# Kernel optimization log

Hardware: AMD Instinct MI355X
Metric: run time of the kernel (lower is better)

## Reference

```python
import jax, jax.numpy as jnp
import numpy as np
from jax import lax

D_MODEL = 96; D_STATE = 16; D_INNER = 192; DT_RANK = 6; K = 4
BSZ = 2; HH = 64; WW = 64


def setup_inputs() -> dict:
    key = jax.random.key(0)
    ks = jax.random.split(key, 16)
    f = lambda k, shape, s=0.02: (jax.random.normal(k, shape) * s).astype(jnp.float32)
    P = DT_RANK + 2 * D_STATE
    return {
        "x": jax.random.normal(ks[0], (BSZ, HH, WW, D_MODEL), jnp.float32),
        "W_in": f(ks[1], (2 * D_INNER, D_MODEL)),
        "b_in": jnp.zeros((2 * D_INNER,), jnp.float32),
        "conv_w": f(ks[2], (D_INNER, 1, 3, 3)),
        "conv_b": jnp.zeros((D_INNER,), jnp.float32),
        "W_xp": f(ks[3], (K * P, K * D_INNER)),
        "b_xp": jnp.zeros((K * P,), jnp.float32),
        "W_dt": f(ks[4], (K * D_INNER, K * DT_RANK)),
        "b_dt": f(ks[5], (K * D_INNER,), 0.1),
        "A_log": jax.random.normal(ks[6], (K * D_INNER, D_STATE), jnp.float32),
        "D_skip": jnp.ones((K * D_INNER,), jnp.float32),
        "dt_bias": jax.random.normal(ks[7], (K * D_INNER,), jnp.float32),
        "W_out": f(ks[8], (D_MODEL, D_INNER)),
        "b_out": jnp.zeros((D_MODEL,), jnp.float32),
        "gamma": jnp.ones((D_INNER,), jnp.float32),
        "beta": jnp.zeros((D_INNER,), jnp.float32),
    }


def cross_scan(x):
    # x: (B, D, H, W) -> (B, 4, D, L); dirs: row-major, col-major, and their reverses
    B, D, H, W = x.shape
    L = H * W
    x0 = x.reshape(B, D, L)
    x1 = jnp.swapaxes(x, 2, 3).reshape(B, D, L)
    return jnp.stack([x0, x1, x0[..., ::-1], x1[..., ::-1]], axis=1)


def cross_merge(ys):
    # ys: (B, 4, D, H, W) -> (B, D, L); inverse of cross_scan, summed
    B, Kk, D, H, W = ys.shape
    L = H * W
    yf = ys.reshape(B, Kk, D, L)
    y02 = yf[:, 0] + yf[:, 2, :, ::-1]
    y13 = yf[:, 1] + yf[:, 3, :, ::-1]
    y13 = jnp.swapaxes(y13.reshape(B, D, W, H), 2, 3).reshape(B, D, L)
    return y02 + y13


def selective_scan(u, dt, A, Bm, Cm, D_skip, dt_bias):
    # u, dt: (B,K,Dv,L); A: (K,Dv,N); Bm, Cm: (B,K,N,L); D_skip, dt_bias: (K,Dv)
    # NOTE: torch code repeats Bm/Cm across Dv; we broadcast instead (same math).
    dt = jax.nn.softplus(dt + dt_bias[None, :, :, None])
    dt_l = jnp.moveaxis(dt, -1, 0)   # (L,B,K,Dv)
    u_l = jnp.moveaxis(u, -1, 0)     # (L,B,K,Dv)
    B_l = jnp.moveaxis(Bm, -1, 0)    # (L,B,K,N)
    C_l = jnp.moveaxis(Cm, -1, 0)    # (L,B,K,N)

    def step(h, inp):
        dt_t, u_t, b_t, c_t = inp
        dA = jnp.exp(dt_t[..., None] * A[None])                 # (B,K,Dv,N)
        dBu = (dt_t * u_t)[..., None] * b_t[:, :, None, :]      # (B,K,Dv,N)
        h = dA * h + dBu
        y = jnp.einsum('bkdn,bkn->bkd', h, c_t)
        return h, y

    h0 = jnp.zeros(u.shape[:3] + (A.shape[-1],), u.dtype)
    _, ys = lax.scan(step, h0, (dt_l, u_l, B_l, C_l))
    ys = jnp.moveaxis(ys, 0, -1)  # (B,K,Dv,L)
    return ys + u * D_skip[None, :, :, None]


def reference(x, W_in, b_in, conv_w, conv_b, W_xp, b_xp, W_dt, b_dt,
              A_log, D_skip, dt_bias, W_out, b_out, gamma, beta):
    B, H, W, _ = x.shape
    L = H * W
    xz = x @ W_in.T + b_in
    xx, z = jnp.split(xz, 2, axis=-1)
    z = jax.nn.silu(z)
    xc = jnp.transpose(xx, (0, 3, 1, 2))  # (B, D, H, W)
    xc = lax.conv_general_dilated(xc, conv_w, (1, 1), 'SAME',
                                  feature_group_count=D_INNER,
                                  dimension_numbers=('NCHW', 'OIHW', 'NCHW'))
    xc = jax.nn.silu(xc + conv_b[None, :, None, None])

    xs = cross_scan(xc)                      # (B, K, D, L)
    xs_flat = xs.reshape(B, K * D_INNER, L)

    x_dbl = jnp.einsum('bcl,pc->bpl', xs_flat, W_xp) + b_xp[None, :, None]
    x_dbl = x_dbl.reshape(B, K, DT_RANK + 2 * D_STATE, L)
    dts, Bm, Cm = jnp.split(x_dbl, [DT_RANK, DT_RANK + D_STATE], axis=2)
    dts = dts.reshape(B, K * DT_RANK, L)
    dts = jnp.einsum('brl,dr->bdl', dts, W_dt) + b_dt[None, :, None]

    A = -jnp.exp(A_log).reshape(K, D_INNER, D_STATE)
    u = xs_flat.reshape(B, K, D_INNER, L)
    dt = dts.reshape(B, K, D_INNER, L)
    ys = selective_scan(u, dt, A, Bm, Cm,
                        D_skip.reshape(K, D_INNER), dt_bias.reshape(K, D_INNER))

    y = cross_merge(ys.reshape(B, K, D_INNER, H, W))  # (B, D, L)
    y = jnp.transpose(y.reshape(B, D_INNER, H, W), (0, 2, 3, 1))

    mu = jnp.mean(y, axis=-1, keepdims=True)
    var = jnp.mean(jnp.square(y - mu), axis=-1, keepdims=True)
    y = (y - mu) * lax.rsqrt(var + 1e-5) * gamma + beta
    y = y * z
    return y @ W_out.T + b_out
```

## Files before the change

kernel.cpp:

```cpp
#include <hip/hip_runtime.h>
#include <cstdint>
#include <cstddef>


#define CHUNK 16
#define NCK   256

#if __has_builtin(__builtin_amdgcn_exp2f)
#define EXP2(x) __builtin_amdgcn_exp2f(x)
#else
#define EXP2(x) exp2f(x)
#endif
#define LOG2E 1.44269504088896340736f
#define LN2   0.69314718055994530942f

typedef __attribute__((ext_vector_type(8))) short short8;
typedef __attribute__((ext_vector_type(8))) unsigned short ushort8;
typedef __attribute__((ext_vector_type(4))) float f32x4;

__device__ __forceinline__ float siluf(float x){ return x * (1.f/(1.f+__expf(-x))); }
__device__ __forceinline__ float softplus_fast(float v){
  float e  = EXP2(v*LOG2E);
  float sp = LN2*__log2f(1.f + e);
  return (v > 20.f) ? v : sp;
}
__device__ __forceinline__ unsigned short f2b(float f){
  uint32_t u = __float_as_uint(f);
  uint32_t r = (u + 0x7fffu + ((u>>16)&1u)) >> 16;
  return (unsigned short)r;
}
__device__ __forceinline__ short8 cast8(const float* p){
  float4 f0 = *(const float4*)p;
  float4 f1 = *(const float4*)(p+4);
  unsigned short t[8] = {f2b(f0.x),f2b(f0.y),f2b(f0.z),f2b(f0.w),
                         f2b(f1.x),f2b(f1.y),f2b(f1.z),f2b(f1.w)};
  return *(short8*)t;
}

__global__ __launch_bounds__(256) void k_pack(
    const float* __restrict__ Wxp, const float* __restrict__ Win,
    const float* __restrict__ Wout,
    unsigned short* __restrict__ Wf, unsigned short* __restrict__ Wfin,
    unsigned short* __restrict__ Wfout)
{
  int tid = blockIdx.x*256 + threadIdx.x;
  int lane = tid & 63;
  int n = lane & 15, q = lane >> 4;
  if (tid < 18432){
    int rest = tid >> 6;
    int pt = rest % 6; rest /= 6;
    int k32 = rest & 3; rest >>= 2;
    int kc = rest % 6; int ph = rest / 6;
    int p = ph*96 + pt*16 + n;
    int kbase = kc*128 + k32*32 + q*8;
    unsigned short v[8];
#pragma unroll
    for (int j = 0; j < 8; j++)
      v[j] = (p < 152) ? f2b(Wxp[(size_t)p*768 + kbase + j]) : (unsigned short)0;
    *(ushort8*)(Wf + (size_t)tid*8) = *(ushort8*)v;
  } else if (tid < 23040){
    int e = tid - 18432;
    int rest = e >> 6;
    int nt = rest % 24, k32 = rest / 24;
    int p = nt*16 + n;
    int kbase = k32*32 + q*8;
    unsigned short v[8];
#pragma unroll
    for (int j = 0; j < 8; j++) v[j] = f2b(Win[(size_t)p*96 + kbase + j]);
    *(ushort8*)(Wfin + (size_t)e*8) = *(ushort8*)v;
  } else if (tid < 25344){
    int e = tid - 23040;
    int rest = e >> 6;
    int nt = rest % 6, k32 = rest / 6;
    int p = nt*16 + n;
    int kbase = k32*32 + q*8;
    unsigned short v[8];
#pragma unroll
    for (int j = 0; j < 8; j++) v[j] = f2b(Wout[(size_t)p*192 + kbase + j]);
    *(ushort8*)(Wfout + (size_t)e*8) = *(ushort8*)v;
  }
}

__global__ __launch_bounds__(256) void k_gemm_in(
    const float* __restrict__ x, const unsigned short* __restrict__ Wfin,
    const float* __restrict__ bias, float* __restrict__ xx, float* __restrict__ zs)
{
  const int tid = threadIdx.x;
  const int lane = tid & 63, w = tid >> 6;
  const int m0 = blockIdx.x*64;
  const int n = lane & 15, q = lane >> 4;
  f32x4 acc[4][6] = {};
#pragma unroll
  for (int k32 = 0; k32 < 3; k32++){
    int kb = k32*32 + q*8;
    short8 a[4];
#pragma unroll
    for (int mf = 0; mf < 4; mf++)
      a[mf] = cast8(x + (size_t)(m0 + mf*16 + n)*96 + kb);
#pragma unroll
    for (int j = 0; j < 6; j++){
      int nt = w*6 + j;
      short8 bfr = *(const short8*)(Wfin + ((size_t)(k32*24 + nt)*64 + lane)*8);
#pragma unroll
      for (int mf = 0; mf < 4; mf++)
        acc[mf][j] = __builtin_amdgcn_mfma_f32_16x16x32_bf16(a[mf], bfr, acc[mf][j], 0, 0, 0);
    }
  }
#pragma unroll
  for (int mf = 0; mf < 4; mf++)
#pragma unroll
    for (int j = 0; j < 6; j++){
      int nn = w*96 + j*16 + n;
      float bv = bias[nn];
#pragma unroll
      for (int reg = 0; reg < 4; reg++){
        int l = m0 + mf*16 + q*4 + reg;
        float v = acc[mf][j][reg] + bv;
        if (nn < 192) xx[(size_t)l*192 + nn] = v;
        else          zs[(size_t)l*192 + (nn-192)] = siluf(v);
      }
    }
}

__global__ __launch_bounds__(256) void k_conv(
    const float* __restrict__ xx, const float* __restrict__ cw, const float* __restrict__ cb,
    float* __restrict__ xc,
    unsigned short* __restrict__ xcb, unsigned short* __restrict__ xcTb)
{
  int gid = blockIdx.x*256 + threadIdx.x;
  int c = gid % 192;
  int l = (gid/192) & 4095;
  int b = gid / (192*4096);
  int h = l >> 6, w = l & 63;
  float s = 0.f;
#pragma unroll
  for (int kh = 0; kh < 3; kh++){
    int h2 = h + kh - 1;
    if ((unsigned)h2 >= 64u) continue;
#pragma unroll
    for (int kw = 0; kw < 3; kw++){
      int w2 = w + kw - 1;
      if ((unsigned)w2 >= 64u) continue;
      s += xx[((size_t)b*4096 + h2*64 + w2)*192 + c] * cw[c*9 + kh*3 + kw];
    }
  }
  s = siluf(s + cb[c]);
  unsigned short sb = f2b(s);
  size_t i0 = ((size_t)b*4096 + l)*192 + c;
  xc[i0] = s; xcb[i0] = sb;
  int tl = (l & 63)*64 + (l >> 6);
  xcTb[((size_t)b*4096 + tl)*192 + c] = sb;
}

__global__ __launch_bounds__(256) void k_gemm_xdbl(
    const unsigned short* __restrict__ xcb, const unsigned short* __restrict__ xcTb,
    const unsigned short* __restrict__ Wf, const float* __restrict__ bxp,
    float* __restrict__ xdbl, float* __restrict__ dts_c)
{
  __shared__ unsigned short Bsh[4*6*64*8];
  const int tid = threadIdx.x;
  const int lane = tid & 63, w = tid >> 6;
  const int wl = w & 1, wp = w >> 1;
  const int l0 = blockIdx.x*64, ph = blockIdx.y, b = blockIdx.z;
  const int n = lane & 15, q = lane >> 4;
  f32x4 acc[2][3] = {};
  const unsigned short* slab0 = Wf + (size_t)ph*6*12288;
  for (int kc = 0; kc < 6; kc++){
    __syncthreads();
    const ushort8* srcp = (const ushort8*)(slab0 + (size_t)kc*12288);
#pragma unroll
    for (int t = 0; t < 6; t++) ((ushort8*)Bsh)[tid + t*256] = srcp[tid + t*256];
    __syncthreads();
#pragma unroll
    for (int k32 = 0; k32 < 4; k32++){
      int kk = kc*128 + k32*32;
      int dir = kk/192; int ch = kk%192 + q*8;
      const unsigned short* sp = (dir & 1) ? xcTb : xcb;
      bool rev = (dir >= 2);
      short8 a[2];
#pragma unroll
      for (int mt = 0; mt < 2; mt++){
        int ls = l0 + wl*32 + mt*16 + n;
        int row = rev ? 4095 - ls : ls;
        a[mt] = *(const short8*)(sp + ((size_t)b*4096 + row)*192 + ch);
      }
#pragma unroll
      for (int j = 0; j < 3; j++){
        short8 bfr = *(const short8*)&Bsh[((size_t)(k32*6 + wp*3 + j)*64 + lane)*8];
#pragma unroll
        for (int mt = 0; mt < 2; mt++)
          acc[mt][j] = __builtin_amdgcn_mfma_f32_16x16x32_bf16(a[mt], bfr, acc[mt][j], 0, 0, 0);
      }
    }
  }
#pragma unroll
  for (int mt = 0; mt < 2; mt++)
#pragma unroll
    for (int j = 0; j < 3; j++){
      int p = ph*96 + (wp*3+j)*16 + n;
      if (p < 152){
        int k = p/38, pp = p%38;
        int off = (pp < 6) ? pp : pp + 2;
        float bias = bxp[p];
#pragma unroll
        for (int reg = 0; reg < 4; reg++){
          int l = l0 + wl*32 + mt*16 + q*4 + reg;
          float val = acc[mt][j][reg] + bias;
          xdbl[(((size_t)b*4 + k)*4096 + l)*48 + off] = val;
          if (pp < 6) dts_c[((size_t)b*4096 + l)*24 + k*6 + pp] = val;
        }
      }
    }
}

__global__ __launch_bounds__(256) void k_scanA(
    const float* __restrict__ xc, const float* __restrict__ xdbl,
    const float* __restrict__ dts_c,
    const float* __restrict__ A_log, const float* __restrict__ Wdt,
    const float* __restrict__ bdt, const float* __restrict__ dtbias,
    float* __restrict__ dte, float* __restrict__ Pb, float* __restrict__ Sb)
{
  const int lane = threadIdx.x & 63;
  const int wid  = __builtin_amdgcn_readfirstlane(blockIdx.x*4 + (threadIdx.x >> 6));
  const int ck = wid & (NCK-1); const int g = wid / NCK;
  const int dblk = g % 3; const int bk = g / 3;
  const int k = bk & 3; const int b = bk >> 2;
  const int d = dblk*64 + lane; const int ch = k*192 + d;
  float An[16];
  {
    const float4* ap = (const float4*)(A_log + (size_t)ch*16);
#pragma unroll
    for (int i = 0; i < 4; i++){
      float4 t = ap[i];
      An[4*i+0] = -LOG2E*__expf(t.x); An[4*i+1] = -LOG2E*__expf(t.y);
      An[4*i+2] = -LOG2E*__expf(t.z); An[4*i+3] = -LOG2E*__expf(t.w);
    }
  }
  float Wr[24];
#pragma unroll
  for (int r = 0; r < 24; r++) Wr[r] = Wdt[(size_t)ch*24 + r];
  const float bsum = bdt[ch] + dtbias[ch];
  const int l0 = ck*CHUNK;
  const bool rev = (k >= 2);
  const int tr = k & 1;
  const int T0 = tr ? ((l0 & 63)*64 + (l0 >> 6)) : l0;
  const int rs = tr ? 64 : 1;
  const int row0 = rev ? 4095 - T0 : T0;
  const int rstep = (rev ? -rs : rs)*192;
  const float* up  = xc + ((size_t)b*4096 + row0)*192 + d;
  const float* qc  = dts_c + ((size_t)b*4096 + l0)*24;
  const float* xbc = xdbl + (((size_t)b*4 + k)*4096 + l0)*48;
  float* dtw = dte + (((size_t)b*4 + k)*4096 + l0)*192 + d;
  float h[16];
#pragma unroll
  for (int n = 0; n < 16; n++) h[n] = 0.f;
  float sdt = 0.f;
#pragma unroll 4
  for (int t = 0; t < CHUNK; t++){
    float u  = up[0];
    float4 B0 = *(const float4*)(xbc + 8);
    float4 B1 = *(const float4*)(xbc + 12);
    float4 B2 = *(const float4*)(xbc + 16);
    float4 B3 = *(const float4*)(xbc + 20);
    float Bv[16] = {B0.x,B0.y,B0.z,B0.w, B1.x,B1.y,B1.z,B1.w,
                    B2.x,B2.y,B2.z,B2.w, B3.x,B3.y,B3.z,B3.w};
    float4 q0 = *(const float4*)(qc);
    float4 q1 = *(const float4*)(qc + 4);
    float4 q2 = *(const float4*)(qc + 8);
    float4 q3 = *(const float4*)(qc + 12);
    float4 q4 = *(const float4*)(qc + 16);
    float4 q5 = *(const float4*)(qc + 20);
    float qv[24] = {q0.x,q0.y,q0.z,q0.w, q1.x,q1.y,q1.z,q1.w,
                    q2.x,q2.y,q2.z,q2.w, q3.x,q3.y,q3.z,q3.w,
                    q4.x,q4.y,q4.z,q4.w, q5.x,q5.y,q5.z,q5.w};
    float v0 = bsum, v1 = 0.f, v2 = 0.f, v3 = 0.f;
#pragma unroll
    for (int r = 0; r < 24; r += 4){
      v0 = fmaf(Wr[r+0], qv[r+0], v0);
      v1 = fmaf(Wr[r+1], qv[r+1], v1);
      v2 = fmaf(Wr[r+2], qv[r+2], v2);
      v3 = fmaf(Wr[r+3], qv[r+3], v3);
    }
    float dt = softplus_fast((v0+v1) + (v2+v3));
    dtw[0] = dt;
    float dtu = dt*u;
    sdt += dt;
#pragma unroll
    for (int n = 0; n < 16; n++){
      float dA = EXP2(dt*An[n]);
      h[n] = fmaf(dA, h[n], dtu*Bv[n]);
    }
    qc += 24; xbc += 48; up += rstep; dtw += 192;
  }
  size_t base = ((size_t)wid*16)*64 + lane;
#pragma unroll
  for (int n = 0; n < 16; n++){
    Pb[base + n*64] = EXP2(An[n]*sdt);
    Sb[base + n*64] = h[n];
  }
}

__global__ __launch_bounds__(64) void k_scanB(
    const float* __restrict__ Pb, const float* __restrict__ Sb, float* __restrict__ H0)
{
  int tid = blockIdx.x*64 + threadIdx.x;
  int lane = tid & 63; int n = (tid >> 6) & 15; int g = tid >> 10;
  float h = 0.f;
#pragma unroll 8
  for (int ck = 0; ck < NCK; ck++){
    size_t idx = (((size_t)(g*NCK + ck)*16) + n)*64 + lane;
    H0[idx] = h;
    h = fmaf(Pb[idx], h, Sb[idx]);
  }
}

__global__ __launch_bounds__(256) void k_scanC(
    const float* __restrict__ xc, const float* __restrict__ xdbl,
    const float* __restrict__ A_log, const float* __restrict__ dte,
    const float* __restrict__ Dskip,
    const float* __restrict__ H0, float* __restrict__ ys)
{
  const int lane = threadIdx.x & 63;
  const int wid  = __builtin_amdgcn_readfirstlane(blockIdx.x*4 + (threadIdx.x >> 6));
  const int ck = wid & (NCK-1); const int g = wid / NCK;
  const int dblk = g % 3; const int bk = g / 3;
  const int k = bk & 3; const int b = bk >> 2;
  const int d = dblk*64 + lane; const int ch = k*192 + d;
  float An[16];
  {
    const float4* ap = (const float4*)(A_log + (size_t)ch*16);
#pragma unroll
    for (int i = 0; i < 4; i++){
      float4 t = ap[i];
      An[4*i+0] = -LOG2E*__expf(t.x); An[4*i+1] = -LOG2E*__expf(t.y);
      An[4*i+2] = -LOG2E*__expf(t.z); An[4*i+3] = -LOG2E*__expf(t.w);
    }
  }
  const float Dv = Dskip[ch];
  const int l0 = ck*CHUNK;
  const bool rev = (k >= 2);
  const int tr = k & 1;
  const int T0 = tr ? ((l0 & 63)*64 + (l0 >> 6)) : l0;
  const int rs = tr ? 64 : 1;
  const int row0 = rev ? 4095 - T0 : T0;
  const int rstep = (rev ? -rs : rs)*192;
  const float* up  = xc + ((size_t)b*4096 + row0)*192 + d;
  const float* xbc = xdbl + (((size_t)b*4 + k)*4096 + l0)*48;
  const float* dtp = dte + (((size_t)b*4 + k)*4096 + l0)*192 + d;
  float* ysp = ys + ((size_t)(k*2 + b))*4096*192 + (size_t)row0*192 + d;
  float h[16];
  size_t base = ((size_t)wid*16)*64 + lane;
#pragma unroll
  for (int n = 0; n < 16; n++) h[n] = H0[base + n*64];
#pragma unroll 4
  for (int t = 0; t < CHUNK; t++){
    float u  = up[0];
    float dt = dtp[0];
    float4 B0 = *(const float4*)(xbc + 8);
    float4 B1 = *(const float4*)(xbc + 12);
    float4 B2 = *(const float4*)(xbc + 16);
    float4 B3 = *(const float4*)(xbc + 20);
    float4 C0 = *(const float4*)(xbc + 24);
    float4 C1 = *(const float4*)(xbc + 28);
    float4 C2 = *(const float4*)(xbc + 32);
    float4 C3 = *(const float4*)(xbc + 36);
    float Bv[16] = {B0.x,B0.y,B0.z,B0.w, B1.x,B1.y,B1.z,B1.w,
                    B2.x,B2.y,B2.z,B2.w, B3.x,B3.y,B3.z,B3.w};
    float Cv[16] = {C0.x,C0.y,C0.z,C0.w, C1.x,C1.y,C1.z,C1.w,
                    C2.x,C2.y,C2.z,C2.w, C3.x,C3.y,C3.z,C3.w};
    float dtu = dt*u;
    float y0 = u*Dv, y1 = 0.f;
#pragma unroll
    for (int n = 0; n < 16; n += 2){
      float dA0 = EXP2(dt*An[n]);
      float dA1 = EXP2(dt*An[n+1]);
      h[n]   = fmaf(dA0, h[n],   dtu*Bv[n]);
      h[n+1] = fmaf(dA1, h[n+1], dtu*Bv[n+1]);
      y0 = fmaf(h[n],   Cv[n],   y0);
      y1 = fmaf(h[n+1], Cv[n+1], y1);
    }
    ysp[0] = y0 + y1;
    xbc += 48; dtp += 192; up += rstep; ysp += rstep;
  }
}

__global__ __launch_bounds__(256) void k_ln(
    const float* __restrict__ ys, const float* __restrict__ zs,
    const float* __restrict__ gamma, const float* __restrict__ beta,
    float* __restrict__ yln)
{
  int row = blockIdx.x*4 + (threadIdx.x >> 6);
  int lane = threadIdx.x & 63;
  int b = row >> 12; int l = row & 4095;
  float v[3];
#pragma unroll
  for (int j = 0; j < 3; j++){
    int c = lane + j*64;
    float s = 0.f;
#pragma unroll
    for (int k = 0; k < 4; k++) s += ys[(((size_t)k*2 + b)*4096 + l)*192 + c];
    v[j] = s;
  }
  float tot = v[0] + v[1] + v[2];
#pragma unroll
  for (int o = 1; o < 64; o <<= 1) tot += __shfl_xor(tot, o);
  float mean = tot * (1.f/192.f);
  float d0 = v[0]-mean, d1 = v[1]-mean, d2 = v[2]-mean;
  float vs = d0*d0 + d1*d1 + d2*d2;
#pragma unroll
  for (int o = 1; o < 64; o <<= 1) vs += __shfl_xor(vs, o);
  float rstd = rsqrtf(vs*(1.f/192.f) + 1e-5f);
  float nd[3] = {d0, d1, d2};
#pragma unroll
  for (int j = 0; j < 3; j++){
    int c = lane + j*64;
    float val = nd[j]*rstd*gamma[c] + beta[c];
    val *= zs[(size_t)row*192 + c];
    yln[(size_t)row*192 + c] = val;
  }
}

__global__ __launch_bounds__(256) void k_gemm_out(
    const float* __restrict__ yln, const unsigned short* __restrict__ Wfout,
    const float* __restrict__ bout, float* __restrict__ out)
{
  const int tid = threadIdx.x;
  const int lane = tid & 63, w = tid >> 6;
  const int m0 = blockIdx.x*64 + w*16;
  const int n = lane & 15, q = lane >> 4;
  f32x4 acc[6] = {};
#pragma unroll
  for (int k32 = 0; k32 < 6; k32++){
    int kb = k32*32 + q*8;
    short8 a = cast8(yln + (size_t)(m0 + n)*192 + kb);
#pragma unroll
    for (int j = 0; j < 6; j++){
      short8 bfr = *(const short8*)(Wfout + ((size_t)(k32*6 + j)*64 + lane)*8);
      acc[j] = __builtin_amdgcn_mfma_f32_16x16x32_bf16(a, bfr, acc[j], 0, 0, 0);
    }
  }
#pragma unroll
  for (int j = 0; j < 6; j++){
    int nn = j*16 + n;
    float bv = bout[nn];
#pragma unroll
    for (int reg = 0; reg < 4; reg++){
      int m = m0 + q*4 + reg;
      out[(size_t)m*96 + nn] = acc[j][reg] + bv;
    }
  }
}

extern "C" void kernel_launch(void* const* d_in, const int* in_sizes, int n_in,
                              void* d_out, int out_size, void* d_ws, size_t ws_size,
                              hipStream_t stream)
{
  const float* x      = (const float*)d_in[0];
  const float* W_in   = (const float*)d_in[1];
  const float* b_in   = (const float*)d_in[2];
  const float* conv_w = (const float*)d_in[3];
  const float* conv_b = (const float*)d_in[4];
  const float* W_xp   = (const float*)d_in[5];
  const float* b_xp   = (const float*)d_in[6];
  const float* W_dt   = (const float*)d_in[7];
  const float* b_dt   = (const float*)d_in[8];
  const float* A_log  = (const float*)d_in[9];
  const float* D_skip = (const float*)d_in[10];
  const float* dt_bias= (const float*)d_in[11];
  const float* W_out  = (const float*)d_in[12];
  const float* b_out  = (const float*)d_in[13];
  const float* gamma  = (const float*)d_in[14];
  const float* beta   = (const float*)d_in[15];
  float* out = (float*)d_out;

  float* ws    = (float*)d_ws;
  float* xx    = ws;
  float* zs    = ws + 1572864;
  float* xc    = ws + 3145728;
  float* xdbl  = ws + 4718592;
  float* ysb   = ws + 6291456;
  float* yln   = ws + 12582912;
  float* dte   = ws + 14155776;
  float* Pb    = ws + 20447232;
  float* Sb    = ws + 26738688;
  float* H0    = ws + 33030144;
  float* dts_c = ws + 39321600;
  unsigned short* xcb   = (unsigned short*)(ws + 39518208);
  unsigned short* xcTb  = xcb + 1572864;
  unsigned short* Wf    = (unsigned short*)(ws + 41091072);
  unsigned short* Wfin  = (unsigned short*)(ws + 41164800);
  unsigned short* Wfout = (unsigned short*)(ws + 41183232);

  k_pack     <<<99,             256, 0, stream>>>(W_xp, W_in, W_out, Wf, Wfin, Wfout);
  k_gemm_in  <<<128,            256, 0, stream>>>(x, Wfin, b_in, xx, zs);
  k_conv     <<<6144,           256, 0, stream>>>(xx, conv_w, conv_b, xc, xcb, xcTb);
  k_gemm_xdbl<<<dim3(64, 2, 2), 256, 0, stream>>>(xcb, xcTb, Wf, b_xp, xdbl, dts_c);
  k_scanA    <<<1536,           256, 0, stream>>>(xc, xdbl, dts_c, A_log, W_dt, b_dt, dt_bias, dte, Pb, Sb);
  k_scanB    <<<384,            64,  0, stream>>>(Pb, Sb, H0);
  k_scanC    <<<1536,           256, 0, stream>>>(xc, xdbl, A_log, dte, D_skip, H0, ysb);
  k_ln       <<<2048,           256, 0, stream>>>(ysb, zs, gamma, beta, yln);
  k_gemm_out <<<128,            256, 0, stream>>>(yln, Wfout, b_out, out);
}
```

Measured before the change: 222.0 us.

## Compute local scan output in pass A, correct with decayed carry-in in C, fuse LN+out GEMM

The first scan pass now also produces the chunk-local output y (h starting from zero) plus the D skip term, and stores the running cumulative dt instead of per-step dt. The third pass only adds the carry-in contribution C·(h0·exp(A·cumdt)). It skips the remaining steps of a chunk once that term is provably negligible for every lane, so it no longer re-reads u or recomputes the recurrence. LayerNorm is fused into the output GEMM through shared-memory bf16 tiles, which removes the yln round trip. The trade-offs are a read-modify-write on ys, a heavier pass A with less unrolling, and an early-exit threshold that drops carry-in terms below about 2^-40 relative to the carried state.

```diff
diff --git a/kernel.cpp b/kernel.cpp
--- a/kernel.cpp
+++ b/kernel.cpp
@@ -218,7 +218,9 @@
     const float* __restrict__ dts_c,
     const float* __restrict__ A_log, const float* __restrict__ Wdt,
     const float* __restrict__ bdt, const float* __restrict__ dtbias,
-    float* __restrict__ dte, float* __restrict__ Pb, float* __restrict__ Sb)
+    const float* __restrict__ Dskip,
+    float* __restrict__ sdte, float* __restrict__ Pb, float* __restrict__ Sb,
+    float* __restrict__ ys)
 {
   const int lane = threadIdx.x & 63;
   const int wid  = __builtin_amdgcn_readfirstlane(blockIdx.x*4 + (threadIdx.x >> 6));
@@ -240,6 +242,7 @@
 #pragma unroll
   for (int r = 0; r < 24; r++) Wr[r] = Wdt[(size_t)ch*24 + r];
   const float bsum = bdt[ch] + dtbias[ch];
+  const float Dv = Dskip[ch];
   const int l0 = ck*CHUNK;
   const bool rev = (k >= 2);
   const int tr = k & 1;
@@ -250,112 +253,15 @@
   const float* up  = xc + ((size_t)b*4096 + row0)*192 + d;
   const float* qc  = dts_c + ((size_t)b*4096 + l0)*24;
   const float* xbc = xdbl + (((size_t)b*4 + k)*4096 + l0)*48;
-  float* dtw = dte + (((size_t)b*4 + k)*4096 + l0)*192 + d;
+  float* sdw = sdte + (((size_t)b*4 + k)*4096 + l0)*192 + d;
+  float* ysp = ys + ((size_t)(k*2 + b))*4096*192 + (size_t)row0*192 + d;
   float h[16];
 #pragma unroll
   for (int n = 0; n < 16; n++) h[n] = 0.f;
   float sdt = 0.f;
-#pragma unroll 4
+#pragma unroll 2
   for (int t = 0; t < CHUNK; t++){
     float u  = up[0];
-    float4 B0 = *(const float4*)(xbc + 8);
-    float4 B1 = *(const float4*)(xbc + 12);
-    float4 B2 = *(const float4*)(xbc + 16);
-    float4 B3 = *(const float4*)(xbc + 20);
-    float Bv[16] = {B0.x,B0.y,B0.z,B0.w, B1.x,B1.y,B1.z,B1.w,
-                    B2.x,B2.y,B2.z,B2.w, B3.x,B3.y,B3.z,B3.w};
-    float4 q0 = *(const float4*)(qc);
-    float4 q1 = *(const float4*)(qc + 4);
-    float4 q2 = *(const float4*)(qc + 8);
-    float4 q3 = *(const float4*)(qc + 12);
-    float4 q4 = *(const float4*)(qc + 16);
-    float4 q5 = *(const float4*)(qc + 20);
-    float qv[24] = {q0.x,q0.y,q0.z,q0.w, q1.x,q1.y,q1.z,q1.w,
-                    q2.x,q2.y,q2.z,q2.w, q3.x,q3.y,q3.z,q3.w,
-                    q4.x,q4.y,q4.z,q4.w, q5.x,q5.y,q5.z,q5.w};
-    float v0 = bsum, v1 = 0.f, v2 = 0.f, v3 = 0.f;
-#pragma unroll
-    for (int r = 0; r < 24; r += 4){
-      v0 = fmaf(Wr[r+0], qv[r+0], v0);
-      v1 = fmaf(Wr[r+1], qv[r+1], v1);
-      v2 = fmaf(Wr[r+2], qv[r+2], v2);
-      v3 = fmaf(Wr[r+3], qv[r+3], v3);
-    }
-    float dt = softplus_fast((v0+v1) + (v2+v3));
-    dtw[0] = dt;
-    float dtu = dt*u;
-    sdt += dt;
-#pragma unroll
-    for (int n = 0; n < 16; n++){
-      float dA = EXP2(dt*An[n]);
-      h[n] = fmaf(dA, h[n], dtu*Bv[n]);
-    }
-    qc += 24; xbc += 48; up += rstep; dtw += 192;
-  }
-  size_t base = ((size_t)wid*16)*64 + lane;
-#pragma unroll
-  for (int n = 0; n < 16; n++){
-    Pb[base + n*64] = EXP2(An[n]*sdt);
-    Sb[base + n*64] = h[n];
-  }
-}
-
-__global__ __launch_bounds__(64) void k_scanB(
-    const float* __restrict__ Pb, const float* __restrict__ Sb, float* __restrict__ H0)
-{
-  int tid = blockIdx.x*64 + threadIdx.x;
-  int lane = tid & 63; int n = (tid >> 6) & 15; int g = tid >> 10;
-  float h = 0.f;
-#pragma unroll 8
-  for (int ck = 0; ck < NCK; ck++){
-    size_t idx = (((size_t)(g*NCK + ck)*16) + n)*64 + lane;
-    H0[idx] = h;
-    h = fmaf(Pb[idx], h, Sb[idx]);
-  }
-}
-
-__global__ __launch_bounds__(256) void k_scanC(
-    const float* __restrict__ xc, const float* __restrict__ xdbl,
-    const float* __restrict__ A_log, const float* __restrict__ dte,
-    const float* __restrict__ Dskip,
-    const float* __restrict__ H0, float* __restrict__ ys)
-{
-  const int lane = threadIdx.x & 63;
-  const int wid  = __builtin_amdgcn_readfirstlane(blockIdx.x*4 + (threadIdx.x >> 6));
-  const int ck = wid & (NCK-1); const int g = wid / NCK;
-  const int dblk = g % 3; const int bk = g / 3;
-  const int k = bk & 3; const int b = bk >> 2;
-  const int d = dblk*64 + lane; const int ch = k*192 + d;
-  float An[16];
-  {
-    const float4* ap = (const float4*)(A_log + (size_t)ch*16);
-#pragma unroll
-    for (int i = 0; i < 4; i++){
-      float4 t = ap[i];
-      An[4*i+0] = -LOG2E*__expf(t.x); An[4*i+1] = -LOG2E*__expf(t.y);
-      An[4*i+2] = -LOG2E*__expf(t.z); An[4*i+3] = -LOG2E*__expf(t.w);
-    }
-  }
-  const float Dv = Dskip[ch];
-  const int l0 = ck*CHUNK;
-  const bool rev = (k >= 2);
-  const int tr = k & 1;
-  const int T0 = tr ? ((l0 & 63)*64 + (l0 >> 6)) : l0;
-  const int rs = tr ? 64 : 1;
-  const int row0 = rev ? 4095 - T0 : T0;
-  const int rstep = (rev ? -rs : rs)*192;
-  const float* up  = xc + ((size_t)b*4096 + row0)*192 + d;
-  const float* xbc = xdbl + (((size_t)b*4 + k)*4096 + l0)*48;
-  const float* dtp = dte + (((size_t)b*4 + k)*4096 + l0)*192 + d;
-  float* ysp = ys + ((size_t)(k*2 + b))*4096*192 + (size_t)row0*192 + d;
-  float h[16];
-  size_t base = ((size_t)wid*16)*64 + lane;
-#pragma unroll
-  for (int n = 0; n < 16; n++) h[n] = H0[base + n*64];
-#pragma unroll 4
-  for (int t = 0; t < CHUNK; t++){
-    float u  = up[0];
-    float dt = dtp[0];
     float4 B0 = *(const float4*)(xbc + 8);
     float4 B1 = *(const float4*)(xbc + 12);
     float4 B2 = *(const float4*)(xbc + 16);
@@ -368,6 +274,26 @@
                     B2.x,B2.y,B2.z,B2.w, B3.x,B3.y,B3.z,B3.w};
     float Cv[16] = {C0.x,C0.y,C0.z,C0.w, C1.x,C1.y,C1.z,C1.w,
                     C2.x,C2.y,C2.z,C2.w, C3.x,C3.y,C3.z,C3.w};
+    float4 q0 = *(const float4*)(qc);
+    float4 q1 = *(const float4*)(qc + 4);
+    float4 q2 = *(const float4*)(qc + 8);
+    float4 q3 = *(const float4*)(qc + 12);
+    float4 q4 = *(const float4*)(qc + 16);
+    float4 q5 = *(const float4*)(qc + 20);
+    float qv[24] = {q0.x,q0.y,q0.z,q0.w, q1.x,q1.y,q1.z,q1.w,
+                    q2.x,q2.y,q2.z,q2.w, q3.x,q3.y,q3.z,q3.w,
+                    q4.x,q4.y,q4.z,q4.w, q5.x,q5.y,q5.z,q5.w};
+    float v0 = bsum, v1 = 0.f, v2 = 0.f, v3 = 0.f;
+#pragma unroll
+    for (int r = 0; r < 24; r += 4){
+      v0 = fmaf(Wr[r+0], qv[r+0], v0);
+      v1 = fmaf(Wr[r+1], qv[r+1], v1);
+      v2 = fmaf(Wr[r+2], qv[r+2], v2);
+      v3 = fmaf(Wr[r+3], qv[r+3], v3);
+    }
+    float dt = softplus_fast((v0+v1) + (v2+v3));
+    sdt += dt;
+    sdw[0] = sdt;
     float dtu = dt*u;
     float y0 = u*Dv, y1 = 0.f;
 #pragma unroll
@@ -380,59 +306,141 @@
       y1 = fmaf(h[n+1], Cv[n+1], y1);
     }
     ysp[0] = y0 + y1;
-    xbc += 48; dtp += 192; up += rstep; ysp += rstep;
-  }
-}
-
-__global__ __launch_bounds__(256) void k_ln(
+    qc += 24; xbc += 48; up += rstep; sdw += 192; ysp += rstep;
+  }
+  size_t base = ((size_t)wid*16)*64 + lane;
+#pragma unroll
+  for (int n = 0; n < 16; n++){
+    Pb[base + n*64] = EXP2(An[n]*sdt);
+    Sb[base + n*64] = h[n];
+  }
+}
+
+__global__ __launch_bounds__(64) void k_scanB(
+    const float* __restrict__ Pb, const float* __restrict__ Sb, float* __restrict__ H0)
+{
+  int tid = blockIdx.x*64 + threadIdx.x;
+  int lane = tid & 63; int n = (tid >> 6) & 15; int g = tid >> 10;
+  float h = 0.f;
+#pragma unroll 8
+  for (int ck = 0; ck < NCK; ck++){
+    size_t idx = (((size_t)(g*NCK + ck)*16) + n)*64 + lane;
+    H0[idx] = h;
+    h = fmaf(Pb[idx], h, Sb[idx]);
+  }
+}
+
+__global__ __launch_bounds__(256) void k_scanC(
+    const float* __restrict__ xdbl, const float* __restrict__ A_log,
+    const float* __restrict__ sdte, const float* __restrict__ H0,
+    float* __restrict__ ys)
+{
+  const int lane = threadIdx.x & 63;
+  const int wid  = __builtin_amdgcn_readfirstlane(blockIdx.x*4 + (threadIdx.x >> 6));
+  const int ck = wid & (NCK-1); const int g = wid / NCK;
+  const int dblk = g % 3; const int bk = g / 3;
+  const int k = bk & 3; const int b = bk >> 2;
+  const int d = dblk*64 + lane; const int ch = k*192 + d;
+  float An[16];
+  {
+    const float4* ap = (const float4*)(A_log + (size_t)ch*16);
+#pragma unroll
+    for (int i = 0; i < 4; i++){
+      float4 t = ap[i];
+      An[4*i+0] = -LOG2E*__expf(t.x); An[4*i+1] = -LOG2E*__expf(t.y);
+      An[4*i+2] = -LOG2E*__expf(t.z); An[4*i+3] = -LOG2E*__expf(t.w);
+    }
+  }
+  float h0[16];
+  size_t base = ((size_t)wid*16)*64 + lane;
+  float m = 0.f, maxAn = -1e30f;
+#pragma unroll
+  for (int n = 0; n < 16; n++){
+    h0[n] = H0[base + n*64];
+    m = fmaxf(m, fabsf(h0[n]));
+    maxAn = fmaxf(maxAn, An[n]);
+  }
+  const float thr = -40.f - __log2f(m + 1e-45f);
+  const int l0 = ck*CHUNK;
+  const bool rev = (k >= 2);
+  const int tr = k & 1;
+  const int T0 = tr ? ((l0 & 63)*64 + (l0 >> 6)) : l0;
+  const int rs = tr ? 64 : 1;
+  const int row0 = rev ? 4095 - T0 : T0;
+  const int rstep = (rev ? -rs : rs)*192;
+  const float* xbc = xdbl + (((size_t)b*4 + k)*4096 + l0)*48;
+  const float* sdp = sdte + (((size_t)b*4 + k)*4096 + l0)*192 + d;
+  float* ysp = ys + ((size_t)(k*2 + b))*4096*192 + (size_t)row0*192 + d;
+  for (int t = 0; t < CHUNK; t++){
+    float sdt = sdp[0];
+    if (__all(maxAn*sdt < thr)) break;
+    float4 C0 = *(const float4*)(xbc + 24);
+    float4 C1 = *(const float4*)(xbc + 28);
+    float4 C2 = *(const float4*)(xbc + 32);
+    float4 C3 = *(const float4*)(xbc + 36);
+    float Cv[16] = {C0.x,C0.y,C0.z,C0.w, C1.x,C1.y,C1.z,C1.w,
+                    C2.x,C2.y,C2.z,C2.w, C3.x,C3.y,C3.z,C3.w};
+    float c0 = 0.f, c1 = 0.f;
+#pragma unroll
+    for (int n = 0; n < 16; n += 2){
+      float e0 = EXP2(An[n]*sdt);
+      float e1 = EXP2(An[n+1]*sdt);
+      c0 = fmaf(h0[n]*e0,   Cv[n],   c0);
+      c1 = fmaf(h0[n+1]*e1, Cv[n+1], c1);
+    }
+    ysp[0] += c0 + c1;
+    xbc += 48; sdp += 192; ysp += rstep;
+  }
+}
+
+__global__ __launch_bounds__(256) void k_lnout(
     const float* __restrict__ ys, const float* __restrict__ zs,
     const float* __restrict__ gamma, const float* __restrict__ beta,
-    float* __restrict__ yln)
-{
-  int row = blockIdx.x*4 + (threadIdx.x >> 6);
-  int lane = threadIdx.x & 63;
-  int b = row >> 12; int l = row & 4095;
-  float v[3];
-#pragma unroll
-  for (int j = 0; j < 3; j++){
-    int c = lane + j*64;
-    float s = 0.f;
-#pragma unroll
-    for (int k = 0; k < 4; k++) s += ys[(((size_t)k*2 + b)*4096 + l)*192 + c];
-    v[j] = s;
-  }
-  float tot = v[0] + v[1] + v[2];
-#pragma unroll
-  for (int o = 1; o < 64; o <<= 1) tot += __shfl_xor(tot, o);
-  float mean = tot * (1.f/192.f);
-  float d0 = v[0]-mean, d1 = v[1]-mean, d2 = v[2]-mean;
-  float vs = d0*d0 + d1*d1 + d2*d2;
-#pragma unroll
-  for (int o = 1; o < 64; o <<= 1) vs += __shfl_xor(vs, o);
-  float rstd = rsqrtf(vs*(1.f/192.f) + 1e-5f);
-  float nd[3] = {d0, d1, d2};
-#pragma unroll
-  for (int j = 0; j < 3; j++){
-    int c = lane + j*64;
-    float val = nd[j]*rstd*gamma[c] + beta[c];
-    val *= zs[(size_t)row*192 + c];
-    yln[(size_t)row*192 + c] = val;
-  }
-}
-
-__global__ __launch_bounds__(256) void k_gemm_out(
-    const float* __restrict__ yln, const unsigned short* __restrict__ Wfout,
-    const float* __restrict__ bout, float* __restrict__ out)
-{
+    const unsigned short* __restrict__ Wfout, const float* __restrict__ bout,
+    float* __restrict__ out)
+{
+  __shared__ unsigned short Ysh[64][192];
   const int tid = threadIdx.x;
   const int lane = tid & 63, w = tid >> 6;
-  const int m0 = blockIdx.x*64 + w*16;
+  const int m0 = blockIdx.x*64;
+  for (int rr = 0; rr < 16; rr++){
+    int r = w*16 + rr;
+    int row = m0 + r;
+    int b = row >> 12; int l = row & 4095;
+    float v[3];
+#pragma unroll
+    for (int j = 0; j < 3; j++){
+      int c = lane + j*64;
+      float s = 0.f;
+#pragma unroll
+      for (int k = 0; k < 4; k++) s += ys[(((size_t)k*2 + b)*4096 + l)*192 + c];
+      v[j] = s;
+    }
+    float tot = v[0] + v[1] + v[2];
+#pragma unroll
+    for (int o = 1; o < 64; o <<= 1) tot += __shfl_xor(tot, o);
+    float mean = tot * (1.f/192.f);
+    float d0 = v[0]-mean, d1 = v[1]-mean, d2 = v[2]-mean;
+    float vs = d0*d0 + d1*d1 + d2*d2;
+#pragma unroll
+    for (int o = 1; o < 64; o <<= 1) vs += __shfl_xor(vs, o);
+    float rstd = rsqrtf(vs*(1.f/192.f) + 1e-5f);
+    float nd[3] = {d0, d1, d2};
+#pragma unroll
+    for (int j = 0; j < 3; j++){
+      int c = lane + j*64;
+      float val = nd[j]*rstd*gamma[c] + beta[c];
+      val *= zs[(size_t)row*192 + c];
+      Ysh[r][c] = f2b(val);
+    }
+  }
+  __syncthreads();
   const int n = lane & 15, q = lane >> 4;
   f32x4 acc[6] = {};
 #pragma unroll
   for (int k32 = 0; k32 < 6; k32++){
     int kb = k32*32 + q*8;
-    short8 a = cast8(yln + (size_t)(m0 + n)*192 + kb);
+    short8 a = *(const short8*)&Ysh[w*16 + n][kb];
 #pragma unroll
     for (int j = 0; j < 6; j++){
       short8 bfr = *(const short8*)(Wfout + ((size_t)(k32*6 + j)*64 + lane)*8);
@@ -445,8 +453,8 @@
     float bv = bout[nn];
 #pragma unroll
     for (int reg = 0; reg < 4; reg++){
-      int m = m0 + q*4 + reg;
-      out[(size_t)m*96 + nn] = acc[j][reg] + bv;
+      int mrow = m0 + w*16 + q*4 + reg;
+      out[(size_t)mrow*96 + nn] = acc[j][reg] + bv;
     }
   }
 }
@@ -479,25 +487,24 @@
   float* xc    = ws + 3145728;
   float* xdbl  = ws + 4718592;
   float* ysb   = ws + 6291456;
-  float* yln   = ws + 12582912;
-  float* dte   = ws + 14155776;
-  float* Pb    = ws + 20447232;
-  float* Sb    = ws + 26738688;
-  float* H0    = ws + 33030144;
-  float* dts_c = ws + 39321600;
-  unsigned short* xcb   = (unsigned short*)(ws + 39518208);
+  float* sdte  = ws + 12582912;
+  float* Pb    = ws + 18874368;
+  float* Sb    = ws + 25165824;
+  float* H0    = ws + 31457280;
+  float* dts_c = ws + 37748736;
+  unsigned short* xcb   = (unsigned short*)(ws + 37945344);
   unsigned short* xcTb  = xcb + 1572864;
-  unsigned short* Wf    = (unsigned short*)(ws + 41091072);
-  unsigned short* Wfin  = (unsigned short*)(ws + 41164800);
-  unsigned short* Wfout = (unsigned short*)(ws + 41183232);
+  unsigned short* Wf    = (unsigned short*)(ws + 39518208);
+  unsigned short* Wfin  = (unsigned short*)(ws + 39591936);
+  unsigned short* Wfout = (unsigned short*)(ws + 39610368);
 
   k_pack     <<<99,             256, 0, stream>>>(W_xp, W_in, W_out, Wf, Wfin, Wfout);
   k_gemm_in  <<<128,            256, 0, stream>>>(x, Wfin, b_in, xx, zs);
   k_conv     <<<6144,           256, 0, stream>>>(xx, conv_w, conv_b, xc, xcb, xcTb);
   k_gemm_xdbl<<<dim3(64, 2, 2), 256, 0, stream>>>(xcb, xcTb, Wf, b_xp, xdbl, dts_c);
-  k_scanA    <<<1536,           256, 0, stream>>>(xc, xdbl, dts_c, A_log, W_dt, b_dt, dt_bias, dte, Pb, Sb);
+  k_scanA    <<<1536,           256, 0, stream>>>(xc, xdbl, dts_c, A_log, W_dt, b_dt, dt_bias,
+                                                  D_skip, sdte, Pb, Sb, ysb);
   k_scanB    <<<384,            64,  0, stream>>>(Pb, Sb, H0);
-  k_scanC    <<<1536,           256, 0, stream>>>(xc, xdbl, A_log, dte, D_skip, H0, ysb);
-  k_ln       <<<2048,           256, 0, stream>>>(ysb, zs, gamma, beta, yln);
-  k_gemm_out <<<128,            256, 0, stream>>>(yln, Wfout, b_out, out);
-}
+  k_scanC    <<<1536,           256, 0, stream>>>(xdbl, A_log, sdte, H0, ysb);
+  k_lnout    <<<128,            256, 0, stream>>>(ysb, zs, gamma, beta, Wfout, b_out, out);
+}
```

Result: slower. 232.5 us (+4.7%).

## Move dt projection out of scan into separate bf16 MFMA GEMM kernel

Applied to the files above, without the earlier changes.

The per-channel dt projection (24-wide dot product plus softplus) is moved out of the chunked scan kernel into a new kernel that computes it with bf16 MFMA instructions, using a W_dt matrix pre-packed in k_pack. The scan kernel now just reads the precomputed dt from memory. This removes scalar FMA work and register pressure from the latency-bound scan loop. In exchange it adds a kernel launch, bf16 rounding of the dt inputs and weights, and an extra full read of the dte buffer in scanA that previously only wrote it.

```diff
diff --git a/kernel.cpp b/kernel.cpp
--- a/kernel.cpp
+++ b/kernel.cpp
@@ -39,9 +39,9 @@
 
 __global__ __launch_bounds__(256) void k_pack(
     const float* __restrict__ Wxp, const float* __restrict__ Win,
-    const float* __restrict__ Wout,
+    const float* __restrict__ Wout, const float* __restrict__ Wdt,
     unsigned short* __restrict__ Wf, unsigned short* __restrict__ Wfin,
-    unsigned short* __restrict__ Wfout)
+    unsigned short* __restrict__ Wfout, unsigned short* __restrict__ Wdtf)
 {
   int tid = blockIdx.x*256 + threadIdx.x;
   int lane = tid & 63;
@@ -78,6 +78,17 @@
 #pragma unroll
     for (int j = 0; j < 8; j++) v[j] = f2b(Wout[(size_t)p*192 + kbase + j]);
     *(ushort8*)(Wfout + (size_t)e*8) = *(ushort8*)v;
+  } else if (tid < 28416){
+    int e = tid - 25344;
+    int nt = e >> 6;
+    int ch = nt*16 + n;
+    unsigned short v[8];
+#pragma unroll
+    for (int j = 0; j < 8; j++){
+      int kk = q*8 + j;
+      v[j] = (kk < 24) ? f2b(Wdt[(size_t)ch*24 + kk]) : (unsigned short)0;
+    }
+    *(ushort8*)(Wdtf + (size_t)e*8) = *(ushort8*)v;
   }
 }
 
@@ -213,12 +224,44 @@
     }
 }
 
+__global__ __launch_bounds__(256) void k_gemm_dt(
+    const float* __restrict__ dts_c, const unsigned short* __restrict__ Wdtf,
+    const float* __restrict__ bdt, const float* __restrict__ dtbias,
+    float* __restrict__ dte)
+{
+  const int tid = threadIdx.x;
+  const int lane = tid & 63, w = tid >> 6;
+  const int m0 = blockIdx.x*64 + w*16;
+  const int kdir = blockIdx.y;
+  const int n = lane & 15, q = lane >> 4;
+  short8 a;
+  if (q < 3) a = cast8(dts_c + (size_t)(m0 + n)*24 + q*8);
+  else { unsigned short z[8] = {0,0,0,0,0,0,0,0}; a = *(short8*)z; }
+  f32x4 acc[12] = {};
+#pragma unroll
+  for (int j = 0; j < 12; j++){
+    int nt = kdir*12 + j;
+    short8 bfr = *(const short8*)(Wdtf + ((size_t)nt*64 + lane)*8);
+    acc[j] = __builtin_amdgcn_mfma_f32_16x16x32_bf16(a, bfr, acc[j], 0, 0, 0);
+  }
+#pragma unroll
+  for (int j = 0; j < 12; j++){
+    int c = j*16 + n;
+    int ch = kdir*192 + c;
+    float bsum = bdt[ch] + dtbias[ch];
+#pragma unroll
+    for (int reg = 0; reg < 4; reg++){
+      int m = m0 + q*4 + reg;
+      int b = m >> 12, l = m & 4095;
+      dte[(((size_t)b*4 + kdir)*4096 + l)*192 + c] = softplus_fast(acc[j][reg] + bsum);
+    }
+  }
+}
+
 __global__ __launch_bounds__(256) void k_scanA(
     const float* __restrict__ xc, const float* __restrict__ xdbl,
-    const float* __restrict__ dts_c,
-    const float* __restrict__ A_log, const float* __restrict__ Wdt,
-    const float* __restrict__ bdt, const float* __restrict__ dtbias,
-    float* __restrict__ dte, float* __restrict__ Pb, float* __restrict__ Sb)
+    const float* __restrict__ A_log, const float* __restrict__ dte,
+    float* __restrict__ Pb, float* __restrict__ Sb)
 {
   const int lane = threadIdx.x & 63;
   const int wid  = __builtin_amdgcn_readfirstlane(blockIdx.x*4 + (threadIdx.x >> 6));
@@ -236,10 +279,6 @@
       An[4*i+2] = -LOG2E*__expf(t.z); An[4*i+3] = -LOG2E*__expf(t.w);
     }
   }
-  float Wr[24];
-#pragma unroll
-  for (int r = 0; r < 24; r++) Wr[r] = Wdt[(size_t)ch*24 + r];
-  const float bsum = bdt[ch] + dtbias[ch];
   const int l0 = ck*CHUNK;
   const bool rev = (k >= 2);
   const int tr = k & 1;
@@ -248,9 +287,8 @@
   const int row0 = rev ? 4095 - T0 : T0;
   const int rstep = (rev ? -rs : rs)*192;
   const float* up  = xc + ((size_t)b*4096 + row0)*192 + d;
-  const float* qc  = dts_c + ((size_t)b*4096 + l0)*24;
   const float* xbc = xdbl + (((size_t)b*4 + k)*4096 + l0)*48;
-  float* dtw = dte + (((size_t)b*4 + k)*4096 + l0)*192 + d;
+  const float* dtp = dte + (((size_t)b*4 + k)*4096 + l0)*192 + d;
   float h[16];
 #pragma unroll
   for (int n = 0; n < 16; n++) h[n] = 0.f;
@@ -258,31 +296,13 @@
 #pragma unroll 4
   for (int t = 0; t < CHUNK; t++){
     float u  = up[0];
+    float dt = dtp[0];
     float4 B0 = *(const float4*)(xbc + 8);
     float4 B1 = *(const float4*)(xbc + 12);
     float4 B2 = *(const float4*)(xbc + 16);
     float4 B3 = *(const float4*)(xbc + 20);
     float Bv[16] = {B0.x,B0.y,B0.z,B0.w, B1.x,B1.y,B1.z,B1.w,
                     B2.x,B2.y,B2.z,B2.w, B3.x,B3.y,B3.z,B3.w};
-    float4 q0 = *(const float4*)(qc);
-    float4 q1 = *(const float4*)(qc + 4);
-    float4 q2 = *(const float4*)(qc + 8);
-    float4 q3 = *(const float4*)(qc + 12);
-    float4 q4 = *(const float4*)(qc + 16);
-    float4 q5 = *(const float4*)(qc + 20);
-    float qv[24] = {q0.x,q0.y,q0.z,q0.w, q1.x,q1.y,q1.z,q1.w,
-                    q2.x,q2.y,q2.z,q2.w, q3.x,q3.y,q3.z,q3.w,
-                    q4.x,q4.y,q4.z,q4.w, q5.x,q5.y,q5.z,q5.w};
-    float v0 = bsum, v1 = 0.f, v2 = 0.f, v3 = 0.f;
-#pragma unroll
-    for (int r = 0; r < 24; r += 4){
-      v0 = fmaf(Wr[r+0], qv[r+0], v0);
-      v1 = fmaf(Wr[r+1], qv[r+1], v1);
-      v2 = fmaf(Wr[r+2], qv[r+2], v2);
-      v3 = fmaf(Wr[r+3], qv[r+3], v3);
-    }
-    float dt = softplus_fast((v0+v1) + (v2+v3));
-    dtw[0] = dt;
     float dtu = dt*u;
     sdt += dt;
 #pragma unroll
@@ -290,7 +310,7 @@
       float dA = EXP2(dt*An[n]);
       h[n] = fmaf(dA, h[n], dtu*Bv[n]);
     }
-    qc += 24; xbc += 48; up += rstep; dtw += 192;
+    xbc += 48; dtp += 192; up += rstep;
   }
   size_t base = ((size_t)wid*16)*64 + lane;
 #pragma unroll
@@ -479,25 +499,27 @@
   float* xc    = ws + 3145728;
   float* xdbl  = ws + 4718592;
   float* ysb   = ws + 6291456;
-  float* yln   = ws + 12582912;
-  float* dte   = ws + 14155776;
-  float* Pb    = ws + 20447232;
-  float* Sb    = ws + 26738688;
-  float* H0    = ws + 33030144;
-  float* dts_c = ws + 39321600;
-  unsigned short* xcb   = (unsigned short*)(ws + 39518208);
+  float* dte   = ws + 12582912;
+  float* Pb    = ws + 18874368;
+  float* Sb    = ws + 25165824;
+  float* H0    = ws + 31457280;
+  float* dts_c = ws + 37748736;
+  unsigned short* xcb   = (unsigned short*)(ws + 37945344);
   unsigned short* xcTb  = xcb + 1572864;
-  unsigned short* Wf    = (unsigned short*)(ws + 41091072);
-  unsigned short* Wfin  = (unsigned short*)(ws + 41164800);
-  unsigned short* Wfout = (unsigned short*)(ws + 41183232);
-
-  k_pack     <<<99,             256, 0, stream>>>(W_xp, W_in, W_out, Wf, Wfin, Wfout);
-  k_gemm_in  <<<128,            256, 0, stream>>>(x, Wfin, b_in, xx, zs);
-  k_conv     <<<6144,           256, 0, stream>>>(xx, conv_w, conv_b, xc, xcb, xcTb);
-  k_gemm_xdbl<<<dim3(64, 2, 2), 256, 0, stream>>>(xcb, xcTb, Wf, b_xp, xdbl, dts_c);
-  k_scanA    <<<1536,           256, 0, stream>>>(xc, xdbl, dts_c, A_log, W_dt, b_dt, dt_bias, dte, Pb, Sb);
-  k_scanB    <<<384,            64,  0, stream>>>(Pb, Sb, H0);
-  k_scanC    <<<1536,           256, 0, stream>>>(xc, xdbl, A_log, dte, D_skip, H0, ysb);
-  k_ln       <<<2048,           256, 0, stream>>>(ysb, zs, gamma, beta, yln);
-  k_gemm_out <<<128,            256, 0, stream>>>(yln, Wfout, b_out, out);
-}
+  unsigned short* Wf    = (unsigned short*)(ws + 39518208);
+  unsigned short* Wfin  = (unsigned short*)(ws + 39591936);
+  unsigned short* Wfout = (unsigned short*)(ws + 39610368);
+  unsigned short* Wdtf  = (unsigned short*)(ws + 39619584);
+  float* yln   = ws + 39631872;
+
+  k_pack     <<<111,             256, 0, stream>>>(W_xp, W_in, W_out, W_dt, Wf, Wfin, Wfout, Wdtf);
+  k_gemm_in  <<<128,             256, 0, stream>>>(x, Wfin, b_in, xx, zs);
+  k_conv     <<<6144,            256, 0, stream>>>(xx, conv_w, conv_b, xc, xcb, xcTb);
+  k_gemm_xdbl<<<dim3(64, 2, 2),  256, 0, stream>>>(xcb, xcTb, Wf, b_xp, xdbl, dts_c);
+  k_gemm_dt  <<<dim3(128, 4),    256, 0, stream>>>(dts_c, Wdtf, b_dt, dt_bias, dte);
+  k_scanA    <<<1536,            256, 0, stream>>>(xc, xdbl, A_log, dte, Pb, Sb);
+  k_scanB    <<<384,             64,  0, stream>>>(Pb, Sb, H0);
+  k_scanC    <<<1536,            256, 0, stream>>>(xc, xdbl, A_log, dte, D_skip, H0, ysb);
+  k_ln       <<<2048,            256, 0, stream>>>(ysb, zs, gamma, beta, yln);
+  k_gemm_out <<<128,             256, 0, stream>>>(yln, Wfout, b_out, out);
+}
```

Result: no change. 223.6 us (+0.7%).
